# Optimization experiments

Hardware: AMD Instinct MI355X
Metric: run time of the kernel (lower is better)

Reference implementation:

```python
import jax, jax.numpy as jnp
import numpy as np

N_HEADS = 16

def setup_inputs() -> dict:
    key = jax.random.key(0)
    k0, k1, k2 = jax.random.split(key, 3)
    B, T, C = 4, 2048, 1024
    x = jax.random.normal(k0, (B, T, C), dtype=jnp.float32)
    # nn.Linear params: y = x @ W.T + b
    w_qkv = jax.random.normal(k1, (3 * C, C), dtype=jnp.float32) * 0.02
    b_qkv = jnp.zeros((3 * C,), dtype=jnp.float32)
    w_proj = jax.random.normal(k2, (C, C), dtype=jnp.float32) * 0.02
    b_proj = jnp.zeros((C,), dtype=jnp.float32)
    return {"x": x, "w_qkv": w_qkv, "b_qkv": b_qkv, "w_proj": w_proj, "b_proj": b_proj}

def reference(x, w_qkv, b_qkv, w_proj, b_proj):
    B, T, C = x.shape
    H = N_HEADS
    hd = C // H
    qkv = x @ w_qkv.T + b_qkv                      # [B, T, 3C]
    q, k, v = jnp.split(qkv, 3, axis=-1)           # each [B, T, C]
    q = q.reshape(B, T, H, hd).transpose(0, 2, 1, 3)  # [B, H, T, hd]
    k = k.reshape(B, T, H, hd).transpose(0, 2, 1, 3)
    v = v.reshape(B, T, H, hd).transpose(0, 2, 1, 3)
    # note: original scales by emb_dim**-0.5 (C), not head_dim**-0.5
    wei = jnp.einsum("bhqd,bhkd->bhqk", q, k) * (C ** -0.5)  # [B, H, T, T]
    causal = jnp.tril(jnp.ones((T, T), dtype=bool))
    wei = jnp.where(causal, wei, -jnp.inf)
    att = jax.nn.softmax(wei, axis=-1)
    out = jnp.einsum("bhqk,bhkd->bhqd", att, v)    # [B, H, T, hd]
    out = out.transpose(0, 2, 1, 3).reshape(B, T, C)
    return out @ w_proj.T + b_proj
```

## Files before the change

kernel.cpp:

```cpp
#include <hip/hip_runtime.h>
#include <hip/hip_bf16.h>

typedef __bf16 bf16;
typedef __bf16 bf16x8 __attribute__((ext_vector_type(8)));
typedef __bf16 bf16x4 __attribute__((ext_vector_type(4)));
typedef float  f32x4  __attribute__((ext_vector_type(4)));

#define LDS_ASYNC16(g, l)                                            \
  __builtin_amdgcn_global_load_lds(                                  \
      (const __attribute__((address_space(1))) void*)(g),            \
      (__attribute__((address_space(3))) void*)(l), 16, 0, 0)

#define QSCALE 0.04508421995f

__global__ void cvt3_f32_bf16(const float* __restrict__ i0, bf16* __restrict__ o0, int n0,
                              const float* __restrict__ i1, bf16* __restrict__ o1, int n1,
                              const float* __restrict__ i2, bf16* __restrict__ o2, int n2) {
  int i = blockIdx.x * blockDim.x + threadIdx.x;
  const float* in;
  bf16* out;
  if (i < n0) {
    in = i0; out = o0;
  } else if (i < n0 + n1) {
    i -= n0; in = i1; out = o1;
  } else {
    i -= n0 + n1;
    if (i >= n2) return;
    in = i2; out = o2;
  }
  float4 v = ((const float4*)in)[i];
  bf16x4 o = {(bf16)v.x, (bf16)v.y, (bf16)v.z, (bf16)v.w};
  ((bf16x4*)out)[i] = o;
}

template <int MODE>
__global__ __launch_bounds__(256, 4) void gemm_bt(
    const bf16* __restrict__ A, const bf16* __restrict__ B,
    const float* __restrict__ bias, float* __restrict__ outf,
    bf16* __restrict__ oq, bf16* __restrict__ ok, bf16* __restrict__ ov,
    int M, int N, int K) {
  __shared__ __align__(16) bf16 As[2][128 * 32];
  __shared__ __align__(16) bf16 Bs[2][128 * 32];
  const int tid = threadIdx.x;
  const int wave = tid >> 6, lane = tid & 63;
  const int quad = lane >> 4, l15 = lane & 15;
  const int bm = blockIdx.x * 128, bn = blockIdx.y * 128;
  const int wrow = (wave >> 1) << 6, wcol = (wave & 1) << 6;

  f32x4 acc[4][4] = {};

  const int csw = ((tid & 3) ^ ((tid >> 3) & 3)) * 8;
  const bf16* gA = A + (size_t)(bm + (tid >> 2)) * K + csw;
  const bf16* gB = B + (size_t)(bn + (tid >> 2)) * K + csw;
  char* lA = (char*)As + wave * 1024;
  char* lB = (char*)Bs + wave * 1024;
  const size_t K64 = (size_t)K * 64;
  const int KT = K >> 5;

#define ST(kt, cb) do {                                   \
    const bf16* a_ = gA + (size_t)(kt) * 32;              \
    const bf16* b_ = gB + (size_t)(kt) * 32;              \
    LDS_ASYNC16(a_, lA + (cb) * 8192);                    \
    LDS_ASYNC16(a_ + K64, lA + (cb) * 8192 + 4096);       \
    LDS_ASYNC16(b_, lB + (cb) * 8192);                    \
    LDS_ASYNC16(b_ + K64, lB + (cb) * 8192 + 4096);       \
  } while (0)

  ST(0, 0);
  ST(1, 1);
  asm volatile("s_waitcnt vmcnt(4)" ::: "memory");
  __builtin_amdgcn_s_barrier();

  const int gsw = (quad ^ ((l15 >> 1) & 3)) * 16;

#pragma unroll 1
  for (int kt = 0; kt < KT; ++kt) {
    const int c = kt & 1;
    const char* bA = (const char*)As + c * 8192;
    const char* bB = (const char*)Bs + c * 8192;
    bf16x8 af[4], bfr[4];
#pragma unroll
    for (int mi = 0; mi < 4; ++mi)
      af[mi] = *(const bf16x8*)(bA + (wrow + mi * 16 + l15) * 64 + gsw);
#pragma unroll
    for (int ni = 0; ni < 4; ++ni)
      bfr[ni] = *(const bf16x8*)(bB + (wcol + ni * 16 + l15) * 64 + gsw);
    asm volatile("s_waitcnt lgkmcnt(0)" ::: "memory");
    __builtin_amdgcn_s_barrier();
    if (kt + 2 < KT) ST(kt + 2, c);
    __builtin_amdgcn_s_setprio(1);
#pragma unroll
    for (int mi = 0; mi < 4; ++mi)
#pragma unroll
      for (int ni = 0; ni < 4; ++ni)
        acc[mi][ni] = __builtin_amdgcn_mfma_f32_16x16x32_bf16(
            af[mi], bfr[ni], acc[mi][ni], 0, 0, 0);
    __builtin_amdgcn_s_setprio(0);
    if (kt + 1 < KT) {
      if (kt + 2 < KT)
        asm volatile("s_waitcnt vmcnt(4)" ::: "memory");
      else
        asm volatile("s_waitcnt vmcnt(0)" ::: "memory");
      __builtin_amdgcn_s_barrier();
    }
  }
#undef ST

#pragma unroll
  for (int mi = 0; mi < 4; ++mi) {
    const int row0 = bm + wrow + mi * 16 + quad * 4;
#pragma unroll
    for (int ni = 0; ni < 4; ++ni) {
      const int col = bn + wcol + ni * 16 + l15;
      const float bv = bias[col];
      if (MODE == 0) {
#pragma unroll
        for (int r = 0; r < 4; ++r)
          outf[(size_t)(row0 + r) * N + col] = acc[mi][ni][r] + bv;
      } else {
        const int part = col >> 10;
        const int cn = col & 1023, h = cn >> 6, d = cn & 63;
        const int b = row0 >> 11, t0 = row0 & 2047;
        if (part == 2) {
          bf16x4 pk = {(bf16)(acc[mi][ni][0] + bv), (bf16)(acc[mi][ni][1] + bv),
                       (bf16)(acc[mi][ni][2] + bv), (bf16)(acc[mi][ni][3] + bv)};
          *(bf16x4*)(ov + ((size_t)(b * 16 + h) * 64 + d) * 2048 + t0) = pk;
        } else {
          const float sc = part ? 1.0f : QSCALE;
          bf16* dst = (part ? ok : oq) + ((size_t)(b * 16 + h) * 2048 + t0) * 64 + d;
#pragma unroll
          for (int r = 0; r < 4; ++r)
            dst[(size_t)r * 64] = (bf16)((acc[mi][ni][r] + bv) * sc);
        }
      }
    }
  }
}

__global__ __launch_bounds__(256) void flash_attn(
    const bf16* __restrict__ qb, const bf16* __restrict__ kb,
    const bf16* __restrict__ vt, bf16* __restrict__ ob) {
  constexpr int T = 2048;
  __shared__ bf16 Ks[2][64 * 72];
  __shared__ bf16 Vs[2][64 * 72];
  __shared__ float Ls[4][2][4][16];
  const int tid = threadIdx.x, wave = tid >> 6, lane = tid & 63;
  const int quad = lane >> 4, l15 = lane & 15;
  const int bh = blockIdx.x;
  const int b = bh >> 4, h = bh & 15;
  const bf16* qbase = qb + (size_t)bh * T * 64;
  const bf16* kbase = kb + (size_t)bh * T * 64;
  const bf16* vbase = vt + (size_t)bh * 64 * T;
  const int srow = tid >> 3, sc = (tid & 7) * 8;

  const int vp0 = (sc & ~31) | ((sc & 8) << 1) | ((sc & 16) >> 2);

  const int qt = 15 - (int)blockIdx.y;
  const int q0 = qt * 128 + wave * 32;

  bf16x8 qf[2][2];
#pragma unroll
  for (int qi = 0; qi < 2; ++qi)
#pragma unroll
    for (int ks = 0; ks < 2; ++ks)
      qf[qi][ks] = *(const bf16x8*)(qbase + (size_t)(q0 + qi * 16 + l15) * 64 +
                                    ks * 32 + quad * 8);

  f32x4 lsumv[2] = {};
  f32x4 oacc[2][4] = {};

  const int nkt = 2 * qt + 2;
  const int ktp = q0 >> 6;

  {
    uint4 k0 = *(const uint4*)(kbase + (size_t)srow * 64 + sc);
    uint4 k1 = *(const uint4*)(kbase + (size_t)(srow + 32) * 64 + sc);
    uint4 v0 = *(const uint4*)(vbase + (size_t)srow * T + sc);
    uint4 v1 = *(const uint4*)(vbase + (size_t)(srow + 32) * T + sc);
    *(uint4*)&Ks[0][srow * 72 + sc] = k0;
    *(uint4*)&Ks[0][(srow + 32) * 72 + sc] = k1;
    *(uint2*)&Vs[0][srow * 72 + vp0] = make_uint2(v0.x, v0.y);
    *(uint2*)&Vs[0][srow * 72 + vp0 + 8] = make_uint2(v0.z, v0.w);
    *(uint2*)&Vs[0][(srow + 32) * 72 + vp0] = make_uint2(v1.x, v1.y);
    *(uint2*)&Vs[0][(srow + 32) * 72 + vp0 + 8] = make_uint2(v1.z, v1.w);
  }

#pragma unroll 1
  for (int kt = 0; kt < nkt; ++kt) {
    __syncthreads();
    const int cur = kt & 1;
    const bool pre = (kt + 1) < nkt;
    uint4 pk0, pk1, pv0, pv1;
    if (pre) {
      const bf16* kp = kbase + (size_t)(kt + 1) * 64 * 64;
      const bf16* vp = vbase + (kt + 1) * 64;
      pk0 = *(const uint4*)(kp + (size_t)srow * 64 + sc);
      pk1 = *(const uint4*)(kp + (size_t)(srow + 32) * 64 + sc);
      pv0 = *(const uint4*)(vp + (size_t)srow * T + sc);
      pv1 = *(const uint4*)(vp + (size_t)(srow + 32) * T + sc);
    }
    if (kt <= ktp) {
      f32x4 st[4][2];
      __builtin_amdgcn_s_setprio(1);
#pragma unroll
      for (int ki = 0; ki < 4; ++ki) {
        bf16x8 kfa = *(const bf16x8*)&Ks[cur][(ki * 16 + l15) * 72 + quad * 8];
        bf16x8 kfb =
            *(const bf16x8*)&Ks[cur][(ki * 16 + l15) * 72 + 32 + quad * 8];
#pragma unroll
        for (int qi = 0; qi < 2; ++qi) {
          f32x4 a = {0.f, 0.f, 0.f, 0.f};
          a = __builtin_amdgcn_mfma_f32_16x16x32_bf16(kfa, qf[qi][0], a, 0, 0, 0);
          a = __builtin_amdgcn_mfma_f32_16x16x32_bf16(kfb, qf[qi][1], a, 0, 0, 0);
          st[ki][qi] = a;
        }
      }
      __builtin_amdgcn_s_setprio(0);
      if (kt == ktp) {
#pragma unroll
        for (int ki = 0; ki < 4; ++ki)
#pragma unroll
          for (int qi = 0; qi < 2; ++qi)
#pragma unroll
            for (int r = 0; r < 4; ++r) {
              const int kcol = kt * 64 + ki * 16 + quad * 4 + r;
              const int qrow = q0 + qi * 16 + l15;
              if (kcol > qrow) st[ki][qi][r] = -__builtin_inff();
            }
      }
#pragma unroll
      for (int ki = 0; ki < 4; ++ki)
#pragma unroll
        for (int qi = 0; qi < 2; ++qi) {
#pragma unroll
          for (int r = 0; r < 4; ++r)
            st[ki][qi][r] = __builtin_amdgcn_exp2f(st[ki][qi][r]);
          lsumv[qi] += st[ki][qi];
        }
      bf16x8 pa8[2][2];
#pragma unroll
      for (int ki2 = 0; ki2 < 2; ++ki2)
#pragma unroll
        for (int qi = 0; qi < 2; ++qi) {
          bf16x8 p;
#pragma unroll
          for (int r = 0; r < 4; ++r) {
            p[r] = (bf16)st[2 * ki2][qi][r];
            p[r + 4] = (bf16)st[2 * ki2 + 1][qi][r];
          }
          pa8[ki2][qi] = p;
        }
      __builtin_amdgcn_s_setprio(1);
#pragma unroll
      for (int di = 0; di < 4; ++di)
#pragma unroll
        for (int ki2 = 0; ki2 < 2; ++ki2) {
          bf16x8 vv = *(const bf16x8*)&Vs[cur][(di * 16 + l15) * 72 + ki2 * 32 +
                                              quad * 8];
#pragma unroll
          for (int qi = 0; qi < 2; ++qi)
            oacc[qi][di] = __builtin_amdgcn_mfma_f32_16x16x32_bf16(
                pa8[ki2][qi], vv, oacc[qi][di], 0, 0, 0);
        }
      __builtin_amdgcn_s_setprio(0);
    }
    if (pre) {
      const int nxt = cur ^ 1;
      *(uint4*)&Ks[nxt][srow * 72 + sc] = pk0;
      *(uint4*)&Ks[nxt][(srow + 32) * 72 + sc] = pk1;
      *(uint2*)&Vs[nxt][srow * 72 + vp0] = make_uint2(pv0.x, pv0.y);
      *(uint2*)&Vs[nxt][srow * 72 + vp0 + 8] = make_uint2(pv0.z, pv0.w);
      *(uint2*)&Vs[nxt][(srow + 32) * 72 + vp0] = make_uint2(pv1.x, pv1.y);
      *(uint2*)&Vs[nxt][(srow + 32) * 72 + vp0 + 8] = make_uint2(pv1.z, pv1.w);
    }
  }

#pragma unroll
  for (int qi = 0; qi < 2; ++qi)
    Ls[wave][qi][quad][l15] =
        lsumv[qi][0] + lsumv[qi][1] + lsumv[qi][2] + lsumv[qi][3];
#pragma unroll
  for (int qi = 0; qi < 2; ++qi)
#pragma unroll
    for (int r = 0; r < 4; ++r) {
      const int rloc = quad * 4 + r;
      const float l = Ls[wave][qi][0][rloc] + Ls[wave][qi][1][rloc] +
                      Ls[wave][qi][2][rloc] + Ls[wave][qi][3][rloc];
      const float inv = 1.f / l;
      const int t = q0 + qi * 16 + rloc;
#pragma unroll
      for (int di = 0; di < 4; ++di) {
        const int d = di * 16 + l15;
        ob[((size_t)b * 2048 + t) * 1024 + h * 64 + d] =
            (bf16)(oacc[qi][di][r] * inv);
      }
    }
}

extern "C" void kernel_launch(void* const* d_in, const int* in_sizes, int n_in,
                              void* d_out, int out_size, void* d_ws,
                              size_t ws_size, hipStream_t stream) {
  const float* x = (const float*)d_in[0];
  const float* w_qkv = (const float*)d_in[1];
  const float* b_qkv = (const float*)d_in[2];
  const float* w_proj = (const float*)d_in[3];
  const float* b_proj = (const float*)d_in[4];
  float* out = (float*)d_out;

  const int B = 4, T = 2048, C = 1024;
  const size_t nx = (size_t)B * T * C;

  char* ws = (char*)d_ws;
  bf16* xb = (bf16*)ws;      ws += nx * 2;
  bf16* wqkvb = (bf16*)ws;   ws += (size_t)3 * C * C * 2;
  bf16* wprojb = (bf16*)ws;  ws += (size_t)C * C * 2;
  bf16* qb = (bf16*)ws;      ws += nx * 2;
  bf16* kbuf = (bf16*)ws;    ws += nx * 2;
  bf16* vtb = (bf16*)ws;     ws += nx * 2;
  bf16* attb = (bf16*)ws;    ws += nx * 2;

  const int n0 = (int)(nx / 4), n1 = 3 * C * C / 4, n2 = C * C / 4;
  cvt3_f32_bf16<<<(n0 + n1 + n2 + 255) / 256, 256, 0, stream>>>(
      x, xb, n0, w_qkv, wqkvb, n1, w_proj, wprojb, n2);

  dim3 g1(64, 24);
  gemm_bt<1><<<g1, 256, 0, stream>>>(xb, wqkvb, b_qkv, nullptr, qb, kbuf, vtb,
                                     B * T, 3 * C, C);
  dim3 g2(64, 16);
  flash_attn<<<g2, 256, 0, stream>>>(qb, kbuf, vtb, attb);

  dim3 g3(64, 8);
  gemm_bt<0><<<g3, 256, 0, stream>>>(attb, wprojb, b_proj, out, nullptr,
                                     nullptr, nullptr, B * T, C, C);
}
```

Baseline: 242.6 us.

## Load GEMM B operand directly from global into registers, bypassing LDS

The B tile is no longer staged through shared memory. Each wave now loads its own B fragments straight from global memory into registers, double-buffered in two register sets, with the loop unrolled by two so each iteration alternates between the sets. Only A still goes through async LDS copies, which halves LDS traffic and footprint. In exchange, B rows are fetched redundantly by the two waves sharing a column block, the reads are less coalesced, register pressure rises, and launch bounds drop from 4 to 3 blocks per CU.

```diff
diff --git a/kernel.cpp b/kernel.cpp
--- a/kernel.cpp
+++ b/kernel.cpp
@@ -10,6 +10,8 @@
   __builtin_amdgcn_global_load_lds(                                  \
       (const __attribute__((address_space(1))) void*)(g),            \
       (__attribute__((address_space(3))) void*)(l), 16, 0, 0)
+
+#define MFENCE asm volatile("" ::: "memory")
 
 #define QSCALE 0.04508421995f
 
@@ -34,13 +36,12 @@
 }
 
 template <int MODE>
-__global__ __launch_bounds__(256, 4) void gemm_bt(
+__global__ __launch_bounds__(256, 3) void gemm_bt(
     const bf16* __restrict__ A, const bf16* __restrict__ B,
     const float* __restrict__ bias, float* __restrict__ outf,
     bf16* __restrict__ oq, bf16* __restrict__ ok, bf16* __restrict__ ov,
     int M, int N, int K) {
   __shared__ __align__(16) bf16 As[2][128 * 32];
-  __shared__ __align__(16) bf16 Bs[2][128 * 32];
   const int tid = threadIdx.x;
   const int wave = tid >> 6, lane = tid & 63;
   const int quad = lane >> 4, l15 = lane & 15;
@@ -51,60 +52,80 @@
 
   const int csw = ((tid & 3) ^ ((tid >> 3) & 3)) * 8;
   const bf16* gA = A + (size_t)(bm + (tid >> 2)) * K + csw;
-  const bf16* gB = B + (size_t)(bn + (tid >> 2)) * K + csw;
   char* lA = (char*)As + wave * 1024;
-  char* lB = (char*)Bs + wave * 1024;
   const size_t K64 = (size_t)K * 64;
   const int KT = K >> 5;
 
-#define ST(kt, cb) do {                                   \
+#define ST_A(kt, cb) do {                                 \
     const bf16* a_ = gA + (size_t)(kt) * 32;              \
-    const bf16* b_ = gB + (size_t)(kt) * 32;              \
     LDS_ASYNC16(a_, lA + (cb) * 8192);                    \
     LDS_ASYNC16(a_ + K64, lA + (cb) * 8192 + 4096);       \
-    LDS_ASYNC16(b_, lB + (cb) * 8192);                    \
-    LDS_ASYNC16(b_ + K64, lB + (cb) * 8192 + 4096);       \
   } while (0)
 
-  ST(0, 0);
-  ST(1, 1);
-  asm volatile("s_waitcnt vmcnt(4)" ::: "memory");
+  const bf16* gB0 = B + (size_t)(bn + wcol + 0 + l15) * K + quad * 8;
+  const bf16* gB1 = B + (size_t)(bn + wcol + 16 + l15) * K + quad * 8;
+  const bf16* gB2 = B + (size_t)(bn + wcol + 32 + l15) * K + quad * 8;
+  const bf16* gB3 = B + (size_t)(bn + wcol + 48 + l15) * K + quad * 8;
+
+#define LB(dst, kt) do {                                              \
+    dst[0] = *(const bf16x8*)(gB0 + (size_t)(kt) * 32);               \
+    dst[1] = *(const bf16x8*)(gB1 + (size_t)(kt) * 32);               \
+    dst[2] = *(const bf16x8*)(gB2 + (size_t)(kt) * 32);               \
+    dst[3] = *(const bf16x8*)(gB3 + (size_t)(kt) * 32);               \
+  } while (0)
+
+  bf16x8 be[4], bo[4];
+
+  ST_A(0, 0);
+  ST_A(1, 1);
+  MFENCE;
+  LB(be, 0);
+  LB(bo, 1);
+  asm volatile("s_waitcnt vmcnt(0)" ::: "memory");
   __builtin_amdgcn_s_barrier();
+  MFENCE;
 
   const int gsw = (quad ^ ((l15 >> 1) & 3)) * 16;
 
+#define BODY(kt, breg) do {                                               \
+    const char* bA_ = (const char*)As + ((kt) & 1) * 8192;                \
+    bf16x8 af[4];                                                         \
+    _Pragma("unroll")                                                     \
+    for (int mi = 0; mi < 4; ++mi)                                        \
+      af[mi] = *(const bf16x8*)(bA_ + (wrow + mi * 16 + l15) * 64 + gsw); \
+    asm volatile("s_waitcnt lgkmcnt(0)" ::: "memory");                    \
+    __builtin_amdgcn_s_barrier();                    \
+    MFENCE;                                 \
+    if ((kt) + 2 < KT) ST_A((kt) + 2, (kt) & 1);                          \
+    MFENCE;                                       \
+    __builtin_amdgcn_s_setprio(1);                                        \
+    _Pragma("unroll")                                                     \
+    for (int mi = 0; mi < 4; ++mi)                                        \
+      _Pragma("unroll")                                                   \
+      for (int ni = 0; ni < 4; ++ni)                                      \
+        acc[mi][ni] = __builtin_amdgcn_mfma_f32_16x16x32_bf16(            \
+            af[mi], breg[ni], acc[mi][ni], 0, 0, 0);                      \
+    __builtin_amdgcn_s_setprio(0);                                        \
+    if ((kt) + 2 < KT) LB(breg, (kt) + 2);          \
+    MFENCE;                                                               \
+    if ((kt) + 1 < KT) {                                                  \
+      if ((kt) + 2 < KT)                                                  \
+        asm volatile("s_waitcnt vmcnt(6)" ::: "memory");                  \
+      else                                                                \
+        asm volatile("s_waitcnt vmcnt(0)" ::: "memory");                  \
+      __builtin_amdgcn_s_barrier();          \
+      MFENCE;                               \
+    }                                                                     \
+  } while (0)
+
 #pragma unroll 1
-  for (int kt = 0; kt < KT; ++kt) {
-    const int c = kt & 1;
-    const char* bA = (const char*)As + c * 8192;
-    const char* bB = (const char*)Bs + c * 8192;
-    bf16x8 af[4], bfr[4];
-#pragma unroll
-    for (int mi = 0; mi < 4; ++mi)
-      af[mi] = *(const bf16x8*)(bA + (wrow + mi * 16 + l15) * 64 + gsw);
-#pragma unroll
-    for (int ni = 0; ni < 4; ++ni)
-      bfr[ni] = *(const bf16x8*)(bB + (wcol + ni * 16 + l15) * 64 + gsw);
-    asm volatile("s_waitcnt lgkmcnt(0)" ::: "memory");
-    __builtin_amdgcn_s_barrier();
-    if (kt + 2 < KT) ST(kt + 2, c);
-    __builtin_amdgcn_s_setprio(1);
-#pragma unroll
-    for (int mi = 0; mi < 4; ++mi)
-#pragma unroll
-      for (int ni = 0; ni < 4; ++ni)
-        acc[mi][ni] = __builtin_amdgcn_mfma_f32_16x16x32_bf16(
-            af[mi], bfr[ni], acc[mi][ni], 0, 0, 0);
-    __builtin_amdgcn_s_setprio(0);
-    if (kt + 1 < KT) {
-      if (kt + 2 < KT)
-        asm volatile("s_waitcnt vmcnt(4)" ::: "memory");
-      else
-        asm volatile("s_waitcnt vmcnt(0)" ::: "memory");
-      __builtin_amdgcn_s_barrier();
-    }
-  }
-#undef ST
+  for (int kt = 0; kt < KT; kt += 2) {
+    BODY(kt, be);
+    BODY(kt + 1, bo);
+  }
+#undef BODY
+#undef LB
+#undef ST_A
 
 #pragma unroll
   for (int mi = 0; mi < 4; ++mi) {
```

After: 300.9 us. +24.0%, slower.

## Use 128x192 six-wave tile for QKV projection GEMM

Applied to the files above, without the earlier changes.

Adds a new GEMM variant with a 128x192 block tile and six waves per block (384 threads), arranged 2x3 over the output, and uses it for the QKV projection. The grid shrinks from 64x24 to 64x16 blocks. A tiles are loaded only by the first four waves while all six load B. The aim is more reuse of each loaded A tile per block and fewer blocks overall, at the cost of more LDS per block and uneven load work across waves.

```diff
diff --git a/kernel.cpp b/kernel.cpp
--- a/kernel.cpp
+++ b/kernel.cpp
@@ -31,6 +31,120 @@
   float4 v = ((const float4*)in)[i];
   bf16x4 o = {(bf16)v.x, (bf16)v.y, (bf16)v.z, (bf16)v.w};
   ((bf16x4*)out)[i] = o;
+}
+
+template <int MODE>
+__global__ __launch_bounds__(384, 6) void gemm_bt6(
+    const bf16* __restrict__ A, const bf16* __restrict__ B,
+    const float* __restrict__ bias, float* __restrict__ outf,
+    bf16* __restrict__ oq, bf16* __restrict__ ok, bf16* __restrict__ ov,
+    int M, int N, int K) {
+  __shared__ __align__(16) bf16 As[2][128 * 32];
+  __shared__ __align__(16) bf16 Bs[2][192 * 32];
+  const int tid = threadIdx.x;
+  const int wave = tid >> 6, lane = tid & 63;
+  const int quad = lane >> 4, l15 = lane & 15;
+  const int bm = blockIdx.x * 128, bn = blockIdx.y * 192;
+  const int wm = wave / 3, wn = wave - wm * 3;
+  const int wrow = wm * 64, wcol = wn * 64;
+
+  f32x4 acc[4][4] = {};
+
+  const int csw = ((lane & 3) ^ ((lane >> 3) & 3)) * 8;
+  const int srow = wave * 32 + (lane >> 2);
+  const bf16* gAst = A + (size_t)(bm + srow) * K + csw;
+  const bf16* gBst = B + (size_t)(bn + srow) * K + csw;
+  char* lA = (char*)As + wave * 2048;
+  char* lB = (char*)Bs + wave * 2048;
+  const size_t K16 = (size_t)K * 16;
+  const int KT = K >> 5;
+
+#define ST(kt, cb) do {                                     \
+    const bf16* b_ = gBst + (size_t)(kt) * 32;              \
+    LDS_ASYNC16(b_,       lB + (cb) * 12288);               \
+    LDS_ASYNC16(b_ + K16, lB + (cb) * 12288 + 1024);        \
+    if (wave < 4) {                                         \
+      const bf16* a_ = gAst + (size_t)(kt) * 32;            \
+      LDS_ASYNC16(a_,       lA + (cb) * 8192);              \
+      LDS_ASYNC16(a_ + K16, lA + (cb) * 8192 + 1024);       \
+    }                                                       \
+  } while (0)
+
+#define WAIT_KEEP1 do {                                                  \
+    if (wave < 4) asm volatile("s_waitcnt vmcnt(4)" ::: "memory");       \
+    else          asm volatile("s_waitcnt vmcnt(2)" ::: "memory");       \
+  } while (0)
+
+  ST(0, 0);
+  ST(1, 1);
+  WAIT_KEEP1;
+  __builtin_amdgcn_s_barrier();
+
+  const int gsw = (quad ^ ((l15 >> 1) & 3)) * 16;
+
+#pragma unroll 1
+  for (int kt = 0; kt < KT; ++kt) {
+    const int c = kt & 1;
+    const char* bA = (const char*)As + c * 8192;
+    const char* bB = (const char*)Bs + c * 12288;
+    bf16x8 af[4], bfr[4];
+#pragma unroll
+    for (int mi = 0; mi < 4; ++mi)
+      af[mi] = *(const bf16x8*)(bA + (wrow + mi * 16 + l15) * 64 + gsw);
+#pragma unroll
+    for (int ni = 0; ni < 4; ++ni)
+      bfr[ni] = *(const bf16x8*)(bB + (wcol + ni * 16 + l15) * 64 + gsw);
+    asm volatile("s_waitcnt lgkmcnt(0)" ::: "memory");
+    __builtin_amdgcn_s_barrier();
+    if (kt + 2 < KT) ST(kt + 2, c);
+    __builtin_amdgcn_s_setprio(1);
+#pragma unroll
+    for (int mi = 0; mi < 4; ++mi)
+#pragma unroll
+      for (int ni = 0; ni < 4; ++ni)
+        acc[mi][ni] = __builtin_amdgcn_mfma_f32_16x16x32_bf16(
+            af[mi], bfr[ni], acc[mi][ni], 0, 0, 0);
+    __builtin_amdgcn_s_setprio(0);
+    if (kt + 1 < KT) {
+      if (kt + 2 < KT)
+        WAIT_KEEP1;
+      else
+        asm volatile("s_waitcnt vmcnt(0)" ::: "memory");
+      __builtin_amdgcn_s_barrier();
+    }
+  }
+#undef ST
+#undef WAIT_KEEP1
+
+#pragma unroll
+  for (int mi = 0; mi < 4; ++mi) {
+    const int row0 = bm + wrow + mi * 16 + quad * 4;
+#pragma unroll
+    for (int ni = 0; ni < 4; ++ni) {
+      const int col = bn + wcol + ni * 16 + l15;
+      const float bv = bias[col];
+      if (MODE == 0) {
+#pragma unroll
+        for (int r = 0; r < 4; ++r)
+          outf[(size_t)(row0 + r) * N + col] = acc[mi][ni][r] + bv;
+      } else {
+        const int part = col >> 10;
+        const int cn = col & 1023, h = cn >> 6, d = cn & 63;
+        const int b = row0 >> 11, t0 = row0 & 2047;
+        if (part == 2) {
+          bf16x4 pk = {(bf16)(acc[mi][ni][0] + bv), (bf16)(acc[mi][ni][1] + bv),
+                       (bf16)(acc[mi][ni][2] + bv), (bf16)(acc[mi][ni][3] + bv)};
+          *(bf16x4*)(ov + ((size_t)(b * 16 + h) * 64 + d) * 2048 + t0) = pk;
+        } else {
+          const float sc = part ? 1.0f : QSCALE;
+          bf16* dst = (part ? ok : oq) + ((size_t)(b * 16 + h) * 2048 + t0) * 64 + d;
+#pragma unroll
+          for (int r = 0; r < 4; ++r)
+            dst[(size_t)r * 64] = (bf16)((acc[mi][ni][r] + bv) * sc);
+        }
+      }
+    }
+  }
 }
 
 template <int MODE>
@@ -323,9 +437,9 @@
   cvt3_f32_bf16<<<(n0 + n1 + n2 + 255) / 256, 256, 0, stream>>>(
       x, xb, n0, w_qkv, wqkvb, n1, w_proj, wprojb, n2);
 
-  dim3 g1(64, 24);
-  gemm_bt<1><<<g1, 256, 0, stream>>>(xb, wqkvb, b_qkv, nullptr, qb, kbuf, vtb,
-                                     B * T, 3 * C, C);
+  dim3 g1(64, 16);
+  gemm_bt6<1><<<g1, 384, 0, stream>>>(xb, wqkvb, b_qkv, nullptr, qb, kbuf, vtb,
+                                      B * T, 3 * C, C);
   dim3 g2(64, 16);
   flash_attn<<<g2, 256, 0, stream>>>(qb, kbuf, vtb, attb);
 
```

Result: slower. 810.3 us (+234.0%).
